# Optimization experiments

Hardware: AMD Instinct MI355X
Metric: run time of the kernel (lower is better)

## Reference

```python
import jax, jax.numpy as jnp
import numpy as np

NUM_HEADS = 12


def setup_inputs() -> dict:
    key = jax.random.key(0)
    k1, k2, k3 = jax.random.split(key, 3)
    B, N, C = 2, 2048, 768
    x = jax.random.normal(k1, (B, N, C), dtype=jnp.float32)
    # xavier_uniform-ish scaled weights
    w_qkv = jax.random.normal(k2, (C, 3 * C), dtype=jnp.float32) * (1.0 / np.sqrt(C))
    w_proj = jax.random.normal(k3, (C, C), dtype=jnp.float32) * (1.0 / np.sqrt(C))
    b_proj = jnp.zeros((C,), dtype=jnp.float32)
    return {"x": x, "w_qkv": w_qkv, "w_proj": w_proj, "b_proj": b_proj}


def reference(x, w_qkv, w_proj, b_proj):
    B, N, C = x.shape
    H = NUM_HEADS
    D = C // H
    scale = D ** -0.5
    # [B, N, 3, H, D]
    qkv = (x @ w_qkv).reshape(B, N, 3, H, D)
    q = qkv[:, :, 0].transpose(0, 2, 1, 3)  # [B, H, N, D]
    k = qkv[:, :, 1].transpose(0, 2, 1, 3)
    v = qkv[:, :, 2].transpose(0, 2, 1, 3)
    attn = jnp.einsum("bhnd,bhmd->bhnm", q, k) * scale  # [B, H, N, N]
    attn = jax.nn.softmax(attn, axis=-1)  # attn_drop = 0.0 -> identity
    out = jnp.einsum("bhnm,bhmd->bhnd", attn, v)  # [B, H, N, D]
    out = out.transpose(0, 2, 1, 3).reshape(B, N, C)
    return out @ w_proj + b_proj  # proj_drop = 0.0 -> identity
```

## Files before the change

kernel.cpp:

```cpp
#include <hip/hip_runtime.h>
#include <hip/hip_bf16.h>

typedef __attribute__((ext_vector_type(8))) short short8;
typedef __attribute__((ext_vector_type(4))) float f32x4;
typedef __attribute__((ext_vector_type(4))) int int4v;

#define HD 64
#define NH 12
#define SEQ 2048
#define CDIM 768

#define QSCALE 0.180336880f

static __device__ __forceinline__ unsigned short f2bf(float f) {
    __hip_bfloat16 h = __float2bfloat16(f);
    return __builtin_bit_cast(unsigned short, h);
}

static __device__ __forceinline__ unsigned cvtpk_bf16(float a, float b) {
    unsigned r;
    asm("v_cvt_pk_bf16_f32 %0, %1, %2" : "=v"(r) : "v"(a), "v"(b));
    return r;
}

#define GLDS16(gp, lp) __builtin_amdgcn_global_load_lds( \
    (const __attribute__((address_space(1))) void*)(gp), \
    (__attribute__((address_space(3))) void*)(lp), 16, 0, 0)

static __device__ __forceinline__ int kperm_f(int r) {
    const int kt = r >> 4, gg = (r >> 2) & 3, jj = r & 3;
    return 32 * (kt & 1) + 8 * gg + 4 * (kt >> 1) + jj;
}

static __device__ __forceinline__ void transpose_tile(const float* __restrict__ in,
        unsigned short* __restrict__ out, int K, int C, int bx, int by,
        float (*t)[33], int tid) {
    const int k0 = bx * 32, c0 = by * 32;
    const int r = tid >> 3, c4 = (tid & 7) * 4;
    const float4 v = *reinterpret_cast<const float4*>(in + (size_t)(k0 + r) * C + c0 + c4);
    t[r][c4 + 0] = v.x; t[r][c4 + 1] = v.y; t[r][c4 + 2] = v.z; t[r][c4 + 3] = v.w;
    __syncthreads();
    ushort4 o;
    o.x = f2bf(t[c4 + 0][r]); o.y = f2bf(t[c4 + 1][r]);
    o.z = f2bf(t[c4 + 2][r]); o.w = f2bf(t[c4 + 3][r]);
    *reinterpret_cast<ushort4*>(out + (size_t)(c0 + r) * K + k0 + c4) = o;
}

__global__ __launch_bounds__(256) void prep_kernel(
        const float* __restrict__ x, const float* __restrict__ wq, const float* __restrict__ wp,
        unsigned short* __restrict__ xb, unsigned short* __restrict__ wqt, unsigned short* __restrict__ wpt) {
    __shared__ float t[32][33];
    const int blk = blockIdx.x, tid = threadIdx.x;
    if (blk < 1728) {
        transpose_tile(wq, wqt, 768, 2304, blk % 24, blk / 24, t, tid);
    } else if (blk < 2304) {
        const int b2 = blk - 1728;
        transpose_tile(wp, wpt, 768, 768, b2 % 24, b2 / 24, t, tid);
    } else {
        const int b3 = blk - 2304;
        #pragma unroll
        for (int it = 0; it < 4; it++) {
            const int i = (b3 * 4 + it) * 256 + tid;
            const float4 v = reinterpret_cast<const float4*>(x)[i];
            ushort4 o;
            o.x = f2bf(v.x); o.y = f2bf(v.y); o.z = f2bf(v.z); o.w = f2bf(v.w);
            reinterpret_cast<ushort4*>(xb)[i] = o;
        }
    }
}

template<int EPI>
__global__ __launch_bounds__(256, 2) void gemm_kernel(
    const unsigned short* __restrict__ A,
    const unsigned short* __restrict__ Bt,
    const int K, const int N,
    unsigned short* __restrict__ Qo, unsigned short* __restrict__ Ko, unsigned short* __restrict__ Vo,
    float* __restrict__ Cout, const float* __restrict__ bias)
{
    const int tid = threadIdx.x;
    const int wave = tid >> 6, lane = tid & 63;
    const int g = lane >> 4, li = lane & 15;
    const int wr = wave >> 1, wc = wave & 1;
    const int m0 = blockIdx.x * 128, n0 = blockIdx.y * 128;

    __shared__ short As[2][128 * 32];
    __shared__ short Bs[2][128 * 32];

    f32x4 acc[4][4];
    #pragma unroll
    for (int i = 0; i < 4; i++)
        #pragma unroll
        for (int j = 0; j < 4; j++)
            acc[i][j] = (f32x4){0.f, 0.f, 0.f, 0.f};

    const int srow = wave * 16 + (lane >> 2);
    const int scol = (lane & 3) * 8;
    const unsigned short* aSrc = A + (size_t)(m0 + srow) * K + scol;
    const unsigned short* bSrc = Bt + (size_t)(n0 + srow) * K + scol;
    const int d0 = wave * 16 * 32, d1 = (wave * 16 + 64) * 32;
    const size_t rowskip = (size_t)64 * K;

    #define GSTAGE(kk, bb) do { \
        GLDS16(aSrc + (kk) * 32,           &As[bb][d0]); \
        GLDS16(aSrc + (kk) * 32 + rowskip, &As[bb][d1]); \
        GLDS16(bSrc + (kk) * 32,           &Bs[bb][d0]); \
        GLDS16(bSrc + (kk) * 32 + rowskip, &Bs[bb][d1]); \
    } while (0)

    const int nk = K >> 5;
    GSTAGE(0, 0);
    asm volatile("s_waitcnt vmcnt(0)\n\ts_barrier" ::: "memory");

    for (int kk = 0; kk < nk; ++kk) {
        const int cb = kk & 1;
        if (kk + 1 < nk) GSTAGE(kk + 1, cb ^ 1);
        const short* Ab = As[cb];
        const short* Bb = Bs[cb];
        short8 af[4], bfr[4];
        #pragma unroll
        for (int mf = 0; mf < 4; mf++)
            af[mf] = *reinterpret_cast<const short8*>(&Ab[(wr * 64 + mf * 16 + li) * 32 + 8 * g]);
        #pragma unroll
        for (int nf = 0; nf < 4; nf++)
            bfr[nf] = *reinterpret_cast<const short8*>(&Bb[(wc * 64 + nf * 16 + li) * 32 + 8 * g]);
        __builtin_amdgcn_s_setprio(1);
        #pragma unroll
        for (int mf = 0; mf < 4; mf++)
            #pragma unroll
            for (int nf = 0; nf < 4; nf++)
                acc[mf][nf] = __builtin_amdgcn_mfma_f32_16x16x32_bf16(af[mf], bfr[nf], acc[mf][nf], 0, 0, 0);
        __builtin_amdgcn_s_setprio(0);
        asm volatile("s_waitcnt vmcnt(0)\n\ts_barrier" ::: "memory");
    }
    #undef GSTAGE

    #pragma unroll
    for (int mf = 0; mf < 4; mf++) {
        #pragma unroll
        for (int nf = 0; nf < 4; nf++) {
            #pragma unroll
            for (int j = 0; j < 4; j++) {
                const int r = m0 + wr * 64 + mf * 16 + 4 * g + j;
                const int c = n0 + wc * 64 + nf * 16 + li;
                const float v = acc[mf][nf][j];
                if (EPI == 0) {
                    const int s = c / 768, rem = c % 768;
                    const int hh = rem >> 6, d = rem & 63;
                    const int bb = r >> 11, n = r & (SEQ - 1);
                    if (s == 0)
                        Qo[(((size_t)bb * NH + hh) * SEQ + n) * HD + d] = f2bf(v * QSCALE);
                    else if (s == 1)
                        Ko[(((size_t)bb * NH + hh) * SEQ + n) * HD + d] = f2bf(v);
                    else
                        Vo[(((size_t)bb * NH + hh) * HD + d) * SEQ + n] = f2bf(v);
                } else {
                    Cout[(size_t)r * N + c] = v + bias[c];
                }
            }
        }
    }
}

__global__ __launch_bounds__(256, 2) void attn_kernel(
    const unsigned short* __restrict__ Q,
    const unsigned short* __restrict__ Kg,
    const unsigned short* __restrict__ Vtg,
    unsigned short* __restrict__ O)
{
    const int tid = threadIdx.x;
    const int wave = tid >> 6, lane = tid & 63;
    const int g = lane >> 4, li = lane & 15;
    const int head = blockIdx.y;
    const int b = head / NH, h = head % NH;
    const int q0 = blockIdx.x * 64 + wave * 16;
    const size_t plane = (size_t)head * SEQ * HD;

    __shared__ short Ks[2][64 * 64];
    __shared__ short Vs[2][64 * 64];

    short8 qf0, qf1;
    {
        const unsigned short* qp = Q + plane + (size_t)(q0 + li) * HD + 8 * g;
        qf0 = *reinterpret_cast<const short8*>(qp);
        qf1 = *reinterpret_cast<const short8*>(qp + 32);
    }
    const short8 ones = {0x3F80, 0x3F80, 0x3F80, 0x3F80, 0x3F80, 0x3F80, 0x3F80, 0x3F80};

    const int lr = lane >> 3;
    const int colS = ((lane & 7) ^ lr) * 8;
    const int rA = wave * 16 + lr;
    const int rB = rA + 8;
    const unsigned short* kSrcA = Kg + plane + (size_t)kperm_f(rA) * HD + colS;
    const unsigned short* kSrcB = Kg + plane + (size_t)kperm_f(rB) * HD + colS;
    const unsigned short* vSrcA = Vtg + plane + (size_t)rA * SEQ + colS;
    const unsigned short* vSrcB = Vtg + plane + (size_t)rB * SEQ + colS;
    const int stA = wave * 1024, stB = stA + 512;

    #define STAGE(kv, bb) do { \
        GLDS16(kSrcA + (size_t)(kv) * HD, &Ks[bb][stA]); \
        GLDS16(kSrcB + (size_t)(kv) * HD, &Ks[bb][stB]); \
        GLDS16(vSrcA + (kv),              &Vs[bb][stA]); \
        GLDS16(vSrcB + (kv),              &Vs[bb][stB]); \
    } while (0)

    f32x4 o_acc[4], l_acc;
    #pragma unroll
    for (int nf = 0; nf < 4; nf++) o_acc[nf] = (f32x4){0.f, 0.f, 0.f, 0.f};
    l_acc = (f32x4){0.f, 0.f, 0.f, 0.f};

    const int sl0 = (g ^ (li & 7)) * 8;
    const int sl1 = ((g + 4) ^ (li & 7)) * 8;

    STAGE(0, 0);
    asm volatile("s_waitcnt vmcnt(0)\n\ts_barrier" ::: "memory");

    for (int it = 0; it < SEQ / 64; ++it) {
        const int cb = it & 1;
        if (it + 1 < SEQ / 64) STAGE((it + 1) * 64, cb ^ 1);
        const short* Kb = Ks[cb];
        const short* Vb = Vs[cb];

        f32x4 s_acc[4];
        #pragma unroll
        for (int kt = 0; kt < 4; kt++) s_acc[kt] = (f32x4){0.f, 0.f, 0.f, 0.f};
        __builtin_amdgcn_s_setprio(1);
        #pragma unroll
        for (int kt = 0; kt < 4; kt++) {
            const short8 ka0 = *reinterpret_cast<const short8*>(&Kb[(16 * kt + li) * 64 + sl0]);
            const short8 ka1 = *reinterpret_cast<const short8*>(&Kb[(16 * kt + li) * 64 + sl1]);
            s_acc[kt] = __builtin_amdgcn_mfma_f32_16x16x32_bf16(ka0, qf0, s_acc[kt], 0, 0, 0);
            s_acc[kt] = __builtin_amdgcn_mfma_f32_16x16x32_bf16(ka1, qf1, s_acc[kt], 0, 0, 0);
        }
        __builtin_amdgcn_s_setprio(0);

        float p[4][4];
        #pragma unroll
        for (int kt = 0; kt < 4; kt++)
            #pragma unroll
            for (int j = 0; j < 4; j++)
                p[kt][j] = exp2f(s_acc[kt][j]);

        const int4v i0 = { (int)cvtpk_bf16(p[0][0], p[0][1]), (int)cvtpk_bf16(p[0][2], p[0][3]),
                           (int)cvtpk_bf16(p[2][0], p[2][1]), (int)cvtpk_bf16(p[2][2], p[2][3]) };
        const int4v i1 = { (int)cvtpk_bf16(p[1][0], p[1][1]), (int)cvtpk_bf16(p[1][2], p[1][3]),
                           (int)cvtpk_bf16(p[3][0], p[3][1]), (int)cvtpk_bf16(p[3][2], p[3][3]) };
        const short8 pa0 = __builtin_bit_cast(short8, i0);
        const short8 pa1 = __builtin_bit_cast(short8, i1);

        __builtin_amdgcn_s_setprio(1);
        l_acc = __builtin_amdgcn_mfma_f32_16x16x32_bf16(ones, pa0, l_acc, 0, 0, 0);
        l_acc = __builtin_amdgcn_mfma_f32_16x16x32_bf16(ones, pa1, l_acc, 0, 0, 0);
        #pragma unroll
        for (int nf = 0; nf < 4; nf++) {
            const short8 va0 = *reinterpret_cast<const short8*>(&Vb[(16 * nf + li) * 64 + sl0]);
            const short8 va1 = *reinterpret_cast<const short8*>(&Vb[(16 * nf + li) * 64 + sl1]);
            o_acc[nf] = __builtin_amdgcn_mfma_f32_16x16x32_bf16(va0, pa0, o_acc[nf], 0, 0, 0);
            o_acc[nf] = __builtin_amdgcn_mfma_f32_16x16x32_bf16(va1, pa1, o_acc[nf], 0, 0, 0);
        }
        __builtin_amdgcn_s_setprio(0);

        asm volatile("s_waitcnt vmcnt(0)\n\ts_barrier" ::: "memory");
    }
    #undef STAGE

    const float inv = 1.0f / l_acc[0];
    unsigned short* dst = O + ((size_t)b * SEQ + q0 + li) * CDIM + h * HD + 4 * g;
    #pragma unroll
    for (int nf = 0; nf < 4; nf++) {
        ushort4 o;
        o.x = f2bf(o_acc[nf][0] * inv);
        o.y = f2bf(o_acc[nf][1] * inv);
        o.z = f2bf(o_acc[nf][2] * inv);
        o.w = f2bf(o_acc[nf][3] * inv);
        *reinterpret_cast<ushort4*>(dst + 16 * nf) = o;
    }
}

extern "C" void kernel_launch(void* const* d_in, const int* in_sizes, int n_in,
                              void* d_out, int out_size, void* d_ws, size_t ws_size,
                              hipStream_t stream) {
    const float* x      = (const float*)d_in[0];
    const float* w_qkv  = (const float*)d_in[1];
    const float* w_proj = (const float*)d_in[2];
    const float* b_proj = (const float*)d_in[3];
    float* out = (float*)d_out;

    char* p = (char*)d_ws;
    auto take = [&](size_t bytes) { char* r = p; p += (bytes + 255) & ~(size_t)255; return r; };
    unsigned short* xb      = (unsigned short*)take((size_t)4096 * 768 * 2);
    unsigned short* wqkv_t  = (unsigned short*)take((size_t)2304 * 768 * 2);
    unsigned short* wproj_t = (unsigned short*)take((size_t)768 * 768 * 2);
    unsigned short* Qb      = (unsigned short*)take((size_t)24 * 2048 * 64 * 2);
    unsigned short* Kb      = (unsigned short*)take((size_t)24 * 2048 * 64 * 2);
    unsigned short* Vb      = (unsigned short*)take((size_t)24 * 2048 * 64 * 2);
    unsigned short* Ob      = (unsigned short*)take((size_t)4096 * 768 * 2);

    prep_kernel<<<3072, 256, 0, stream>>>(x, w_qkv, w_proj, xb, wqkv_t, wproj_t);
    gemm_kernel<0><<<dim3(32, 18), 256, 0, stream>>>(xb, wqkv_t, 768, 2304, Qb, Kb, Vb, nullptr, nullptr);
    attn_kernel<<<dim3(32, 24), 256, 0, stream>>>(Qb, Kb, Vb, Ob);
    gemm_kernel<1><<<dim3(32, 6), 256, 0, stream>>>(Ob, wproj_t, 768, 768, nullptr, nullptr, nullptr, out, b_proj);
}
```

Baseline: 107.4 us.

## Split attention over the KV sequence in two halves and add a combine kernel

The attention kernel is templated on a KV split count. With two splits, each block processes half of the key/value sequence and writes unnormalized fp32 partial outputs and row sums to workspace. A new combine kernel sums the partials, normalizes them and writes bf16 output. The aim is to double the number of blocks so the grid fills the GPU with a smaller wave-quantization tail. In exchange it adds an extra launch and roughly 25 MB of fp32 partial-output traffic, and it only takes this path when the workspace is large enough.

```diff
diff --git a/kernel.cpp b/kernel.cpp
--- a/kernel.cpp
+++ b/kernel.cpp
@@ -161,19 +161,24 @@
     }
 }
 
+template<int NSPLIT>
 __global__ __launch_bounds__(256, 2) void attn_kernel(
     const unsigned short* __restrict__ Q,
     const unsigned short* __restrict__ Kg,
     const unsigned short* __restrict__ Vtg,
-    unsigned short* __restrict__ O)
+    unsigned short* __restrict__ O,
+    float* __restrict__ o_part, float* __restrict__ l_part)
 {
     const int tid = threadIdx.x;
     const int wave = tid >> 6, lane = tid & 63;
     const int g = lane >> 4, li = lane & 15;
     const int head = blockIdx.y;
+    const int split = blockIdx.z;
     const int b = head / NH, h = head % NH;
     const int q0 = blockIdx.x * 64 + wave * 16;
     const size_t plane = (size_t)head * SEQ * HD;
+    const int kvbase = split * (SEQ / NSPLIT);
+    const int niter = SEQ / NSPLIT / 64;
 
     __shared__ short Ks[2][64 * 64];
     __shared__ short Vs[2][64 * 64];
@@ -211,12 +216,12 @@
     const int sl0 = (g ^ (li & 7)) * 8;
     const int sl1 = ((g + 4) ^ (li & 7)) * 8;
 
-    STAGE(0, 0);
+    STAGE(kvbase, 0);
     asm volatile("s_waitcnt vmcnt(0)\n\ts_barrier" ::: "memory");
 
-    for (int it = 0; it < SEQ / 64; ++it) {
+    for (int it = 0; it < niter; ++it) {
         const int cb = it & 1;
-        if (it + 1 < SEQ / 64) STAGE((it + 1) * 64, cb ^ 1);
+        if (it + 1 < niter) STAGE(kvbase + (it + 1) * 64, cb ^ 1);
         const short* Kb = Ks[cb];
         const short* Vb = Vs[cb];
 
@@ -263,16 +268,64 @@
     }
     #undef STAGE
 
-    const float inv = 1.0f / l_acc[0];
-    unsigned short* dst = O + ((size_t)b * SEQ + q0 + li) * CDIM + h * HD + 4 * g;
-    #pragma unroll
-    for (int nf = 0; nf < 4; nf++) {
+    if (NSPLIT == 1) {
+        const float inv = 1.0f / l_acc[0];
+        unsigned short* dst = O + ((size_t)b * SEQ + q0 + li) * CDIM + h * HD + 4 * g;
+        #pragma unroll
+        for (int nf = 0; nf < 4; nf++) {
+            ushort4 o;
+            o.x = f2bf(o_acc[nf][0] * inv);
+            o.y = f2bf(o_acc[nf][1] * inv);
+            o.z = f2bf(o_acc[nf][2] * inv);
+            o.w = f2bf(o_acc[nf][3] * inv);
+            *reinterpret_cast<ushort4*>(dst + 16 * nf) = o;
+        }
+    } else {
+        float* op = o_part + ((((size_t)split * 24 + head) * SEQ) + q0 + li) * HD + 4 * g;
+        #pragma unroll
+        for (int nf = 0; nf < 4; nf++)
+            *reinterpret_cast<f32x4*>(op + 16 * nf) = o_acc[nf];
+        if (g == 0)
+            l_part[((size_t)split * 24 + head) * SEQ + q0 + li] = l_acc[0];
+    }
+}
+
+__global__ __launch_bounds__(256) void combine_kernel(
+    const float* __restrict__ o_part, const float* __restrict__ l_part,
+    unsigned short* __restrict__ O, int nsplit)
+{
+    const int tid = threadIdx.x;
+    const int plane = blockIdx.y;
+    const int b = plane / NH, h = plane % NH;
+    const int q = blockIdx.x * 64 + (tid >> 2);
+    const int dg = (tid & 3) * 16;
+
+    float acc[16];
+    #pragma unroll
+    for (int i = 0; i < 16; i++) acc[i] = 0.f;
+    float l = 0.f;
+    for (int s = 0; s < nsplit; ++s) {
+        const float* base = o_part + (((size_t)s * 24 + plane) * SEQ + q) * HD + dg;
+        #pragma unroll
+        for (int c = 0; c < 4; c++) {
+            const float4 v = *reinterpret_cast<const float4*>(base + c * 4);
+            acc[c * 4 + 0] += v.x; acc[c * 4 + 1] += v.y;
+            acc[c * 4 + 2] += v.z; acc[c * 4 + 3] += v.w;
+        }
+        l += l_part[((size_t)s * 24 + plane) * SEQ + q];
+    }
+    const float inv = 1.0f / l;
+    unsigned short* dst = O + ((size_t)b * SEQ + q) * CDIM + h * HD + dg;
+    #pragma unroll
+    for (int c = 0; c < 2; c++) {
         ushort4 o;
-        o.x = f2bf(o_acc[nf][0] * inv);
-        o.y = f2bf(o_acc[nf][1] * inv);
-        o.z = f2bf(o_acc[nf][2] * inv);
-        o.w = f2bf(o_acc[nf][3] * inv);
-        *reinterpret_cast<ushort4*>(dst + 16 * nf) = o;
+        o.x = f2bf(acc[c * 8 + 0] * inv); o.y = f2bf(acc[c * 8 + 1] * inv);
+        o.z = f2bf(acc[c * 8 + 2] * inv); o.w = f2bf(acc[c * 8 + 3] * inv);
+        ushort4 o2;
+        o2.x = f2bf(acc[c * 8 + 4] * inv); o2.y = f2bf(acc[c * 8 + 5] * inv);
+        o2.z = f2bf(acc[c * 8 + 6] * inv); o2.w = f2bf(acc[c * 8 + 7] * inv);
+        *reinterpret_cast<ushort4*>(dst + c * 8)     = o;
+        *reinterpret_cast<ushort4*>(dst + c * 8 + 4) = o2;
     }
 }
 
@@ -294,9 +347,17 @@
     unsigned short* Kb      = (unsigned short*)take((size_t)24 * 2048 * 64 * 2);
     unsigned short* Vb      = (unsigned short*)take((size_t)24 * 2048 * 64 * 2);
     unsigned short* Ob      = (unsigned short*)take((size_t)4096 * 768 * 2);
+    float* o_part           = (float*)take((size_t)2 * 24 * 2048 * 64 * 4);
+    float* l_part           = (float*)take((size_t)2 * 24 * 2048 * 4);
+    const bool can_split = (size_t)(p - (char*)d_ws) <= ws_size;
 
     prep_kernel<<<3072, 256, 0, stream>>>(x, w_qkv, w_proj, xb, wqkv_t, wproj_t);
     gemm_kernel<0><<<dim3(32, 18), 256, 0, stream>>>(xb, wqkv_t, 768, 2304, Qb, Kb, Vb, nullptr, nullptr);
-    attn_kernel<<<dim3(32, 24), 256, 0, stream>>>(Qb, Kb, Vb, Ob);
+    if (can_split) {
+        attn_kernel<2><<<dim3(32, 24, 2), 256, 0, stream>>>(Qb, Kb, Vb, Ob, o_part, l_part);
+        combine_kernel<<<dim3(32, 24), 256, 0, stream>>>(o_part, l_part, Ob, 2);
+    } else {
+        attn_kernel<1><<<dim3(32, 24, 1), 256, 0, stream>>>(Qb, Kb, Vb, Ob, nullptr, nullptr);
+    }
     gemm_kernel<1><<<dim3(32, 6), 256, 0, stream>>>(Ob, wproj_t, 768, 768, nullptr, nullptr, nullptr, out, b_proj);
 }
```

Result: slower. 113.0 us (+5.2%).

## Load K/V directly from global into registers, drop LDS staging and barriers

Applied to the files above, without the earlier changes.

Replaces the LDS double-buffered K/V staging in the attention kernel with direct per-wave global loads into registers. The next K tile is register-prefetched while the current one is used. The launch becomes a 1D grid remapped so the blocks of each head land on the same XCD for L2 locality, and the occupancy hint is raised to 3 blocks per CU. This removes LDS traffic and the per-tile block barriers, but each wave now fetches K/V itself, so global/L2 traffic rises fourfold and register pressure grows.

```diff
diff --git a/kernel.cpp b/kernel.cpp
--- a/kernel.cpp
+++ b/kernel.cpp
@@ -9,6 +9,7 @@
 #define NH 12
 #define SEQ 2048
 #define CDIM 768
+#define NT (SEQ / 64)
 
 #define QSCALE 0.180336880f
 
@@ -161,7 +162,64 @@
     }
 }
 
-__global__ __launch_bounds__(256, 2) void attn_kernel(
+static __device__ __forceinline__ void attn_iter(
+    const short8 (&cK0)[4], const short8 (&cK1)[4],
+    short8 (&nK0)[4], short8 (&nK1)[4],
+    const unsigned short* kBase, const int (&kOff)[4],
+    const unsigned short* vBase, const int (&vOff)[4],
+    int kv0, int kvn,
+    const short8 qf0, const short8 qf1, const short8 ones,
+    f32x4 (&o_acc)[4], f32x4& l_acc)
+{
+    #pragma unroll
+    for (int kt = 0; kt < 4; kt++) {
+        nK0[kt] = *reinterpret_cast<const short8*>(kBase + kOff[kt] + (size_t)kvn * HD);
+        nK1[kt] = *reinterpret_cast<const short8*>(kBase + kOff[kt] + (size_t)kvn * HD + 32);
+    }
+    short8 v0[4], v1[4];
+    #pragma unroll
+    for (int nf = 0; nf < 4; nf++) {
+        v0[nf] = *reinterpret_cast<const short8*>(vBase + vOff[nf] + kv0);
+        v1[nf] = *reinterpret_cast<const short8*>(vBase + vOff[nf] + kv0 + 32);
+    }
+
+    f32x4 s_acc[4];
+    #pragma unroll
+    for (int kt = 0; kt < 4; kt++) s_acc[kt] = (f32x4){0.f, 0.f, 0.f, 0.f};
+    __builtin_amdgcn_s_setprio(1);
+    #pragma unroll
+    for (int kt = 0; kt < 4; kt++) {
+        s_acc[kt] = __builtin_amdgcn_mfma_f32_16x16x32_bf16(cK0[kt], qf0, s_acc[kt], 0, 0, 0);
+        s_acc[kt] = __builtin_amdgcn_mfma_f32_16x16x32_bf16(cK1[kt], qf1, s_acc[kt], 0, 0, 0);
+    }
+    __builtin_amdgcn_s_setprio(0);
+
+    float p[4][4];
+    #pragma unroll
+    for (int kt = 0; kt < 4; kt++)
+        #pragma unroll
+        for (int j = 0; j < 4; j++)
+            p[kt][j] = exp2f(s_acc[kt][j]);
+
+    const int4v i0 = { (int)cvtpk_bf16(p[0][0], p[0][1]), (int)cvtpk_bf16(p[0][2], p[0][3]),
+                       (int)cvtpk_bf16(p[2][0], p[2][1]), (int)cvtpk_bf16(p[2][2], p[2][3]) };
+    const int4v i1 = { (int)cvtpk_bf16(p[1][0], p[1][1]), (int)cvtpk_bf16(p[1][2], p[1][3]),
+                       (int)cvtpk_bf16(p[3][0], p[3][1]), (int)cvtpk_bf16(p[3][2], p[3][3]) };
+    const short8 pa0 = __builtin_bit_cast(short8, i0);
+    const short8 pa1 = __builtin_bit_cast(short8, i1);
+
+    __builtin_amdgcn_s_setprio(1);
+    l_acc = __builtin_amdgcn_mfma_f32_16x16x32_bf16(ones, pa0, l_acc, 0, 0, 0);
+    l_acc = __builtin_amdgcn_mfma_f32_16x16x32_bf16(ones, pa1, l_acc, 0, 0, 0);
+    #pragma unroll
+    for (int nf = 0; nf < 4; nf++) {
+        o_acc[nf] = __builtin_amdgcn_mfma_f32_16x16x32_bf16(v0[nf], pa0, o_acc[nf], 0, 0, 0);
+        o_acc[nf] = __builtin_amdgcn_mfma_f32_16x16x32_bf16(v1[nf], pa1, o_acc[nf], 0, 0, 0);
+    }
+    __builtin_amdgcn_s_setprio(0);
+}
+
+__global__ __launch_bounds__(256, 3) void attn_kernel(
     const unsigned short* __restrict__ Q,
     const unsigned short* __restrict__ Kg,
     const unsigned short* __restrict__ Vtg,
@@ -170,13 +228,14 @@
     const int tid = threadIdx.x;
     const int wave = tid >> 6, lane = tid & 63;
     const int g = lane >> 4, li = lane & 15;
-    const int head = blockIdx.y;
+
+    const int bid = blockIdx.x;
+    const int xcd = bid & 7, pos = bid >> 3;
+    const int head = xcd * 3 + (pos >> 5);
+    const int qb = pos & 31;
     const int b = head / NH, h = head % NH;
-    const int q0 = blockIdx.x * 64 + wave * 16;
+    const int q0 = qb * 64 + wave * 16;
     const size_t plane = (size_t)head * SEQ * HD;
-
-    __shared__ short Ks[2][64 * 64];
-    __shared__ short Vs[2][64 * 64];
 
     short8 qf0, qf1;
     {
@@ -186,82 +245,35 @@
     }
     const short8 ones = {0x3F80, 0x3F80, 0x3F80, 0x3F80, 0x3F80, 0x3F80, 0x3F80, 0x3F80};
 
-    const int lr = lane >> 3;
-    const int colS = ((lane & 7) ^ lr) * 8;
-    const int rA = wave * 16 + lr;
-    const int rB = rA + 8;
-    const unsigned short* kSrcA = Kg + plane + (size_t)kperm_f(rA) * HD + colS;
-    const unsigned short* kSrcB = Kg + plane + (size_t)kperm_f(rB) * HD + colS;
-    const unsigned short* vSrcA = Vtg + plane + (size_t)rA * SEQ + colS;
-    const unsigned short* vSrcB = Vtg + plane + (size_t)rB * SEQ + colS;
-    const int stA = wave * 1024, stB = stA + 512;
-
-    #define STAGE(kv, bb) do { \
-        GLDS16(kSrcA + (size_t)(kv) * HD, &Ks[bb][stA]); \
-        GLDS16(kSrcB + (size_t)(kv) * HD, &Ks[bb][stB]); \
-        GLDS16(vSrcA + (kv),              &Vs[bb][stA]); \
-        GLDS16(vSrcB + (kv),              &Vs[bb][stB]); \
-    } while (0)
+    const unsigned short* kBase = Kg + plane;
+    const unsigned short* vBase = Vtg + plane;
+    int kOff[4], vOff[4];
+    #pragma unroll
+    for (int kt = 0; kt < 4; kt++) kOff[kt] = kperm_f(16 * kt + li) * HD + 8 * g;
+    #pragma unroll
+    for (int nf = 0; nf < 4; nf++) vOff[nf] = (16 * nf + li) * SEQ + 8 * g;
 
     f32x4 o_acc[4], l_acc;
     #pragma unroll
     for (int nf = 0; nf < 4; nf++) o_acc[nf] = (f32x4){0.f, 0.f, 0.f, 0.f};
     l_acc = (f32x4){0.f, 0.f, 0.f, 0.f};
 
-    const int sl0 = (g ^ (li & 7)) * 8;
-    const int sl1 = ((g + 4) ^ (li & 7)) * 8;
-
-    STAGE(0, 0);
-    asm volatile("s_waitcnt vmcnt(0)\n\ts_barrier" ::: "memory");
-
-    for (int it = 0; it < SEQ / 64; ++it) {
-        const int cb = it & 1;
-        if (it + 1 < SEQ / 64) STAGE((it + 1) * 64, cb ^ 1);
-        const short* Kb = Ks[cb];
-        const short* Vb = Vs[cb];
-
-        f32x4 s_acc[4];
-        #pragma unroll
-        for (int kt = 0; kt < 4; kt++) s_acc[kt] = (f32x4){0.f, 0.f, 0.f, 0.f};
-        __builtin_amdgcn_s_setprio(1);
-        #pragma unroll
-        for (int kt = 0; kt < 4; kt++) {
-            const short8 ka0 = *reinterpret_cast<const short8*>(&Kb[(16 * kt + li) * 64 + sl0]);
-            const short8 ka1 = *reinterpret_cast<const short8*>(&Kb[(16 * kt + li) * 64 + sl1]);
-            s_acc[kt] = __builtin_amdgcn_mfma_f32_16x16x32_bf16(ka0, qf0, s_acc[kt], 0, 0, 0);
-            s_acc[kt] = __builtin_amdgcn_mfma_f32_16x16x32_bf16(ka1, qf1, s_acc[kt], 0, 0, 0);
-        }
-        __builtin_amdgcn_s_setprio(0);
-
-        float p[4][4];
-        #pragma unroll
-        for (int kt = 0; kt < 4; kt++)
-            #pragma unroll
-            for (int j = 0; j < 4; j++)
-                p[kt][j] = exp2f(s_acc[kt][j]);
-
-        const int4v i0 = { (int)cvtpk_bf16(p[0][0], p[0][1]), (int)cvtpk_bf16(p[0][2], p[0][3]),
-                           (int)cvtpk_bf16(p[2][0], p[2][1]), (int)cvtpk_bf16(p[2][2], p[2][3]) };
-        const int4v i1 = { (int)cvtpk_bf16(p[1][0], p[1][1]), (int)cvtpk_bf16(p[1][2], p[1][3]),
-                           (int)cvtpk_bf16(p[3][0], p[3][1]), (int)cvtpk_bf16(p[3][2], p[3][3]) };
-        const short8 pa0 = __builtin_bit_cast(short8, i0);
-        const short8 pa1 = __builtin_bit_cast(short8, i1);
-
-        __builtin_amdgcn_s_setprio(1);
-        l_acc = __builtin_amdgcn_mfma_f32_16x16x32_bf16(ones, pa0, l_acc, 0, 0, 0);
-        l_acc = __builtin_amdgcn_mfma_f32_16x16x32_bf16(ones, pa1, l_acc, 0, 0, 0);
-        #pragma unroll
-        for (int nf = 0; nf < 4; nf++) {
-            const short8 va0 = *reinterpret_cast<const short8*>(&Vb[(16 * nf + li) * 64 + sl0]);
-            const short8 va1 = *reinterpret_cast<const short8*>(&Vb[(16 * nf + li) * 64 + sl1]);
-            o_acc[nf] = __builtin_amdgcn_mfma_f32_16x16x32_bf16(va0, pa0, o_acc[nf], 0, 0, 0);
-            o_acc[nf] = __builtin_amdgcn_mfma_f32_16x16x32_bf16(va1, pa1, o_acc[nf], 0, 0, 0);
-        }
-        __builtin_amdgcn_s_setprio(0);
-
-        asm volatile("s_waitcnt vmcnt(0)\n\ts_barrier" ::: "memory");
-    }
-    #undef STAGE
+    short8 kA0[4], kA1[4], kB0[4], kB1[4];
+    #pragma unroll
+    for (int kt = 0; kt < 4; kt++) {
+        kA0[kt] = *reinterpret_cast<const short8*>(kBase + kOff[kt]);
+        kA1[kt] = *reinterpret_cast<const short8*>(kBase + kOff[kt] + 32);
+    }
+
+    for (int it = 0; it < NT; it += 2) {
+        const int kv0 = it * 64;
+        const int kvn1 = (it + 1) * 64;
+        const int kvn2 = (it + 2 < NT) ? (it + 2) * 64 : (NT - 1) * 64;
+        attn_iter(kA0, kA1, kB0, kB1, kBase, kOff, vBase, vOff,
+                  kv0, kvn1, qf0, qf1, ones, o_acc, l_acc);
+        attn_iter(kB0, kB1, kA0, kA1, kBase, kOff, vBase, vOff,
+                  kvn1, kvn2, qf0, qf1, ones, o_acc, l_acc);
+    }
 
     const float inv = 1.0f / l_acc[0];
     unsigned short* dst = O + ((size_t)b * SEQ + q0 + li) * CDIM + h * HD + 4 * g;
@@ -297,6 +309,6 @@
 
     prep_kernel<<<3072, 256, 0, stream>>>(x, w_qkv, w_proj, xb, wqkv_t, wproj_t);
     gemm_kernel<0><<<dim3(32, 18), 256, 0, stream>>>(xb, wqkv_t, 768, 2304, Qb, Kb, Vb, nullptr, nullptr);
-    attn_kernel<<<dim3(32, 24), 256, 0, stream>>>(Qb, Kb, Vb, Ob);
+    attn_kernel<<<768, 256, 0, stream>>>(Qb, Kb, Vb, Ob);
     gemm_kernel<1><<<dim3(32, 6), 256, 0, stream>>>(Ob, wproj_t, 768, 768, nullptr, nullptr, nullptr, out, b_proj);
 }
```

Result: slower. 232.5 us (+116.5%).

## Triple-buffer LDS staging in GEMM and attention kernels with prefetch depth two

Applied to the files above, without the earlier changes.

Both the GEMM and attention kernels move from double to triple buffering of shared-memory tiles. Two tiles are now kept in flight, and partial vmcnt waits let the loop compute on the current tile while the next two load. Launch bounds rise to three blocks per CU. This aims to hide more global-load latency, at the cost of extra LDS per block and tighter register budgets, which could cause spills or reduce actual occupancy.

```diff
diff --git a/kernel.cpp b/kernel.cpp
--- a/kernel.cpp
+++ b/kernel.cpp
@@ -9,6 +9,7 @@
 #define NH 12
 #define SEQ 2048
 #define CDIM 768
+#define NT (SEQ / 64)
 
 #define QSCALE 0.180336880f
 
@@ -70,7 +71,7 @@
 }
 
 template<int EPI>
-__global__ __launch_bounds__(256, 2) void gemm_kernel(
+__global__ __launch_bounds__(256, 3) void gemm_kernel(
     const unsigned short* __restrict__ A,
     const unsigned short* __restrict__ Bt,
     const int K, const int N,
@@ -83,8 +84,8 @@
     const int wr = wave >> 1, wc = wave & 1;
     const int m0 = blockIdx.x * 128, n0 = blockIdx.y * 128;
 
-    __shared__ short As[2][128 * 32];
-    __shared__ short Bs[2][128 * 32];
+    __shared__ short As[3][128 * 32];
+    __shared__ short Bs[3][128 * 32];
 
     f32x4 acc[4][4];
     #pragma unroll
@@ -109,13 +110,16 @@
 
     const int nk = K >> 5;
     GSTAGE(0, 0);
-    asm volatile("s_waitcnt vmcnt(0)\n\ts_barrier" ::: "memory");
-
+    GSTAGE(1, 1);
+    asm volatile("s_waitcnt vmcnt(4)\n\ts_barrier" ::: "memory");
+
+    int cur = 0;
     for (int kk = 0; kk < nk; ++kk) {
-        const int cb = kk & 1;
-        if (kk + 1 < nk) GSTAGE(kk + 1, cb ^ 1);
-        const short* Ab = As[cb];
-        const short* Bb = Bs[cb];
+        const int sbuf = (cur == 0) ? 2 : cur - 1;
+        const bool stage = (kk + 2 < nk);
+        if (stage) GSTAGE(kk + 2, sbuf);
+        const short* Ab = As[cur];
+        const short* Bb = Bs[cur];
         short8 af[4], bfr[4];
         #pragma unroll
         for (int mf = 0; mf < 4; mf++)
@@ -130,7 +134,9 @@
             for (int nf = 0; nf < 4; nf++)
                 acc[mf][nf] = __builtin_amdgcn_mfma_f32_16x16x32_bf16(af[mf], bfr[nf], acc[mf][nf], 0, 0, 0);
         __builtin_amdgcn_s_setprio(0);
-        asm volatile("s_waitcnt vmcnt(0)\n\ts_barrier" ::: "memory");
+        if (stage) asm volatile("s_waitcnt vmcnt(4)\n\ts_barrier" ::: "memory");
+        else       asm volatile("s_waitcnt vmcnt(0)\n\ts_barrier" ::: "memory");
+        cur = (cur == 2) ? 0 : cur + 1;
     }
     #undef GSTAGE
 
@@ -161,7 +167,7 @@
     }
 }
 
-__global__ __launch_bounds__(256, 2) void attn_kernel(
+__global__ __launch_bounds__(256, 3) void attn_kernel(
     const unsigned short* __restrict__ Q,
     const unsigned short* __restrict__ Kg,
     const unsigned short* __restrict__ Vtg,
@@ -175,8 +181,8 @@
     const int q0 = blockIdx.x * 64 + wave * 16;
     const size_t plane = (size_t)head * SEQ * HD;
 
-    __shared__ short Ks[2][64 * 64];
-    __shared__ short Vs[2][64 * 64];
+    __shared__ short Ks[3][64 * 64];
+    __shared__ short Vs[3][64 * 64];
 
     short8 qf0, qf1;
     {
@@ -212,13 +218,16 @@
     const int sl1 = ((g + 4) ^ (li & 7)) * 8;
 
     STAGE(0, 0);
-    asm volatile("s_waitcnt vmcnt(0)\n\ts_barrier" ::: "memory");
-
-    for (int it = 0; it < SEQ / 64; ++it) {
-        const int cb = it & 1;
-        if (it + 1 < SEQ / 64) STAGE((it + 1) * 64, cb ^ 1);
-        const short* Kb = Ks[cb];
-        const short* Vb = Vs[cb];
+    STAGE(64, 1);
+    asm volatile("s_waitcnt vmcnt(4)\n\ts_barrier" ::: "memory");
+
+    int cur = 0;
+    for (int it = 0; it < NT; ++it) {
+        const int sbuf = (cur == 0) ? 2 : cur - 1;
+        const bool stage = (it + 2 < NT);
+        if (stage) STAGE((it + 2) * 64, sbuf);
+        const short* Kb = Ks[cur];
+        const short* Vb = Vs[cur];
 
         f32x4 s_acc[4];
         #pragma unroll
@@ -259,7 +268,9 @@
         }
         __builtin_amdgcn_s_setprio(0);
 
-        asm volatile("s_waitcnt vmcnt(0)\n\ts_barrier" ::: "memory");
+        if (stage) asm volatile("s_waitcnt vmcnt(4)\n\ts_barrier" ::: "memory");
+        else       asm volatile("s_waitcnt vmcnt(0)\n\ts_barrier" ::: "memory");
+        cur = (cur == 2) ? 0 : cur + 1;
     }
     #undef STAGE
 
```

After: 108.5 us. Within noise of the previous version (+1.0%).
